# Performance work log

Measured on AMD Instinct MI355X. Metric: run time of the kernel, lower is better.

Reference implementation:

```python
import jax, jax.numpy as jnp
import numpy as np

N = 50000      # total nodes across batch of graphs
E = 800000     # total directed edges (avg degree 16)
B = 64         # number of graphs
D = 128        # input_dim == hidden_dim
L = 4          # num_layers - 1 GIN layers
OUT = 10
BN_EPS = 1e-5


def setup_inputs() -> dict:
    key = jax.random.key(0)
    ks = jax.random.split(key, 12)
    s = 0.05
    return {
        "x": jax.random.normal(ks[0], (N, D), jnp.float32),
        "pi": jax.random.uniform(ks[1], (B, 25), jnp.float32),
        "eps": jnp.zeros((L,), jnp.float32),
        "mlp_w1": jax.random.normal(ks[2], (L, D, D), jnp.float32) * s,
        "mlp_b1": jnp.zeros((L, D), jnp.float32),
        "mlp_bn_g": jnp.ones((L, D), jnp.float32),
        "mlp_bn_b": jnp.zeros((L, D), jnp.float32),
        "mlp_w2": jax.random.normal(ks[3], (L, D, D), jnp.float32) * s,
        "mlp_b2": jnp.zeros((L, D), jnp.float32),
        "bn_g": jnp.ones((L, D), jnp.float32),
        "bn_b": jnp.zeros((L, D), jnp.float32),
        "attend_w": jax.random.normal(ks[4], (D * (L + 1), 1), jnp.float32) * s,
        "attend_b": jnp.zeros((1,), jnp.float32),
        "pi_w": jax.random.normal(ks[5], (25, 16), jnp.float32) * s,
        "pi_b": jnp.zeros((16,), jnp.float32),
        "out_w": jax.random.normal(ks[6], (D * (L + 1) + 16, OUT), jnp.float32) * s,
        "out_b": jnp.zeros((OUT,), jnp.float32),
        "edge_index": jax.random.randint(ks[7], (2, E), 0, N, dtype=jnp.int32),
        "graph_id": jnp.sort(jax.random.randint(ks[8], (N,), 0, B, dtype=jnp.int32)),
    }


def _bn(z, g, b):
    # BatchNorm1d in training mode over all nodes (axis 0)
    m = z.mean(axis=0)
    v = z.var(axis=0)
    return (z - m) * jax.lax.rsqrt(v + BN_EPS) * g + b


def reference(x, pi, eps, mlp_w1, mlp_b1, mlp_bn_g, mlp_bn_b, mlp_w2, mlp_b2,
              bn_g, bn_b, attend_w, attend_b, pi_w, pi_b, out_w, out_b,
              edge_index, graph_id):
    src, dst = edge_index[0], edge_index[1]
    h = x
    reps = [x]
    for l in range(L):
        # GIN sum aggregation (learn_eps=True: no self-loops in Adj)
        pooled = jax.ops.segment_sum(h[src], dst, num_segments=N)
        pooled = pooled + (1.0 + eps[l]) * h
        # 2-layer MLP: Linear -> BN -> ReLU -> Linear
        z = jax.nn.relu(_bn(pooled @ mlp_w1[l] + mlp_b1[l], mlp_bn_g[l], mlp_bn_b[l]))
        z = z @ mlp_w2[l] + mlp_b2[l]
        # outer BN + ReLU
        h = jax.nn.relu(_bn(z, bn_g[l], bn_b[l]))
        reps.append(h)
    hr = jnp.concatenate(reps, axis=1)               # [N, D*(L+1)]
    # per-graph attention softmax over nodes
    scores = (hr @ attend_w + attend_b)[:, 0]        # [N]
    smax = jax.ops.segment_max(scores, graph_id, num_segments=B)
    e = jnp.exp(scores - smax[graph_id])
    denom = jax.ops.segment_sum(e, graph_id, num_segments=B)
    coef = e / denom[graph_id]
    gemb = jax.ops.segment_sum(hr * coef[:, None], graph_id, num_segments=B)  # [B, D*(L+1)]
    # persistence-image branch (PI computed host-side; treated as input)
    pie = jax.nn.relu(pi @ pi_w + pi_b)              # [B, 16]
    feat = jnp.concatenate([gemb, pie], axis=1)      # [B, D*(L+1)+16]
    return feat @ out_w + out_b                      # [B, OUT]
```

## Files before the change

### kernel.cpp

```cpp
#include <hip/hip_runtime.h>
#include <hip/hip_bf16.h>

#define NN 50000
#define EE 800000
#define BBG 64
#define DD 128
#define LLAY 4
#define HRW 640
#define NOUT 10
#define SCANB 196

typedef __hip_bfloat16 bf16;
typedef __attribute__((ext_vector_type(8))) short short8;
typedef __attribute__((ext_vector_type(4))) float f32x4;

__device__ __forceinline__ float b2f(bf16 v) { return __bfloat162float(v); }
__device__ __forceinline__ float bflo(unsigned u) { return __uint_as_float(u << 16); }
__device__ __forceinline__ float bfhi(unsigned u) { return __uint_as_float(u & 0xffff0000u); }
__device__ __forceinline__ unsigned short f2bs(float v) {
  bf16 h = __float2bfloat16(v);
  unsigned short r; __builtin_memcpy(&r, &h, 2); return r;
}
__device__ __forceinline__ int dtype_of(const void* __restrict__ bng) {
  return (*(const unsigned*)bng == 0x3F800000u) ? 1 : 0;
}
__device__ __forceinline__ float ldf(const void* __restrict__ p, long i, int dt) {
  return dt ? ((const float*)p)[i] : b2f(((const bf16*)p)[i]);
}

__device__ __forceinline__ int lower_bound_i(const int* __restrict__ a, int n, int key) {
  int lo = 0, hi = n;
  while (lo < hi) { int mid = (lo + hi) >> 1; if (a[mid] < key) lo = mid + 1; else hi = mid; }
  return lo;
}

__global__ __launch_bounds__(256) void gnn_prep_w(const void* __restrict__ w1,
                                                  const void* __restrict__ w2,
                                                  bf16* __restrict__ w1t,
                                                  bf16* __restrict__ w2t,
                                                  const void* __restrict__ bng) {
  int dt = dtype_of(bng);
  int i = blockIdx.x * 256 + threadIdx.x;
  int l = i >> 14, rem = i & 16383, n = rem >> 7, k = rem & 127;
  long src = (long)l * 16384 + k * 128 + n;
  w1t[i] = __float2bfloat16(ldf(w1, src, dt));
  w2t[i] = __float2bfloat16(ldf(w2, src, dt));
}

__global__ __launch_bounds__(256) void gnn_copy_x(const void* __restrict__ x,
                                                  bf16* __restrict__ hrb,
                                                  const void* __restrict__ bng) {
  int dt = dtype_of(bng);
  int idx = blockIdx.x * 256 + threadIdx.x;
  int n = idx >> 6, cu = idx & 63;
  unsigned o;
  if (dt) {
    const float2 v = ((const float2*)x)[idx];
    o = (unsigned)f2bs(v.x) | ((unsigned)f2bs(v.y) << 16);
  } else {
    o = ((const unsigned*)x)[idx];
  }
  *(unsigned*)(hrb + (size_t)n * HRW + 2 * cu) = o;
}

__global__ __launch_bounds__(256) void gnn_hist(const int* __restrict__ ei,
                                                int* __restrict__ counts,
                                                int* __restrict__ rel) {
  int e = blockIdx.x * 256 + threadIdx.x;
  rel[e] = atomicAdd(&counts[ei[EE + e]], 1);
}

__global__ __launch_bounds__(256) void gnn_scan1(const int* __restrict__ counts,
                                                 int* __restrict__ blocksum) {
  __shared__ int buf[256];
  int tid = threadIdx.x;
  int i = blockIdx.x * 256 + tid;
  buf[tid] = (i < NN) ? counts[i] : 0;
  __syncthreads();
  for (int s = 128; s > 0; s >>= 1) {
    if (tid < s) buf[tid] += buf[tid + s];
    __syncthreads();
  }
  if (tid == 0) blocksum[blockIdx.x] = buf[0];
}

__global__ __launch_bounds__(256) void gnn_scan2(const int* __restrict__ blocksum,
                                                 int* __restrict__ blockofs,
                                                 int* __restrict__ rowstart) {
  __shared__ int buf[256];
  int tid = threadIdx.x;
  int v = (tid < SCANB) ? blocksum[tid] : 0;
  buf[tid] = v;
  __syncthreads();
  for (int ofs = 1; ofs < 256; ofs <<= 1) {
    int t = (tid >= ofs) ? buf[tid - ofs] : 0;
    __syncthreads();
    buf[tid] += t;
    __syncthreads();
  }
  blockofs[tid] = buf[tid] - v;
  if (tid == 255) rowstart[NN] = buf[255];
}

__global__ __launch_bounds__(256) void gnn_scan3(const int* __restrict__ counts,
                                                 const int* __restrict__ blockofs,
                                                 int* __restrict__ rowstart) {
  __shared__ int buf[256];
  int tid = threadIdx.x;
  int i = blockIdx.x * 256 + tid;
  int v = (i < NN) ? counts[i] : 0;
  buf[tid] = v;
  __syncthreads();
  for (int ofs = 1; ofs < 256; ofs <<= 1) {
    int t = (tid >= ofs) ? buf[tid - ofs] : 0;
    __syncthreads();
    buf[tid] += t;
    __syncthreads();
  }
  int val = blockofs[blockIdx.x] + buf[tid] - v;
  if (i < NN) rowstart[i] = val;
}

__global__ __launch_bounds__(256) void gnn_fill(const int* __restrict__ ei,
                                                const int* __restrict__ rowstart,
                                                const int* __restrict__ rel,
                                                int* __restrict__ csr_src) {
  int e = blockIdx.x * 256 + threadIdx.x;
  int src = ei[e];
  int dst = ei[EE + e];
  csr_src[rowstart[dst] + rel[e]] = src;
}

__device__ __forceinline__ void acc8(float* a, uint4 u) {
  a[0] += bflo(u.x); a[1] += bfhi(u.x);
  a[2] += bflo(u.y); a[3] += bfhi(u.y);
  a[4] += bflo(u.z); a[5] += bfhi(u.z);
  a[6] += bflo(u.w); a[7] += bfhi(u.w);
}

__device__ __forceinline__ float2 statsum(const float* __restrict__ stat, int c) {
  float s = 0.f, q = 0.f;
  #pragma unroll
  for (int k = 0; k < 8; k++) { s += stat[k * 256 + c]; q += stat[k * 256 + 128 + c]; }
  return make_float2(s, q);
}

__global__ __launch_bounds__(512) void gnn_gmg1(const bf16* __restrict__ hrb, int l,
                                                const int* __restrict__ rowstart,
                                                const int* __restrict__ csr_src,
                                                const void* __restrict__ eps,
                                                const bf16* __restrict__ Wt,
                                                const void* __restrict__ bias, int biasOfs,
                                                bf16* __restrict__ out,
                                                float* __restrict__ statOut,
                                                const void* __restrict__ bng) {
  int dt = dtype_of(bng);
  __shared__ __align__(16) unsigned ar[16][68];
  int tid = threadIdx.x, w = tid >> 6, lane = tid & 63;
  int q = lane >> 4, il = lane & 15;
  int r0 = blockIdx.x * 16;
  const bf16* stripe = hrb + l * DD;
  float s = 1.0f + ldf(eps, l, dt);

  #pragma unroll
  for (int i = 2 * w; i < 2 * w + 2; i++) {
    int n = r0 + i;
    float a[8] = {0.f, 0.f, 0.f, 0.f, 0.f, 0.f, 0.f, 0.f};
    if (q == 0) {
      uint4 u = *(const uint4*)(stripe + (size_t)n * HRW + il * 8);
      a[0] = s * bflo(u.x); a[1] = s * bfhi(u.x);
      a[2] = s * bflo(u.y); a[3] = s * bfhi(u.y);
      a[4] = s * bflo(u.z); a[5] = s * bfhi(u.z);
      a[6] = s * bflo(u.w); a[7] = s * bfhi(u.w);
    }
    int start = rowstart[n], end = rowstart[n + 1];
    for (int base = start; base < end; base += 64) {
      int m = end - base; if (m > 64) m = 64;
      int idx = (base + lane < end) ? csr_src[base + lane] : 0;
      int j = 0;
      for (; j + 16 <= m; j += 16) {
        int s0 = __shfl(idx, j + q, 64);
        int s1 = __shfl(idx, j + 4 + q, 64);
        int s2 = __shfl(idx, j + 8 + q, 64);
        int s3 = __shfl(idx, j + 12 + q, 64);
        uint4 u0 = *(const uint4*)(stripe + (size_t)s0 * HRW + il * 8);
        uint4 u1 = *(const uint4*)(stripe + (size_t)s1 * HRW + il * 8);
        uint4 u2 = *(const uint4*)(stripe + (size_t)s2 * HRW + il * 8);
        uint4 u3 = *(const uint4*)(stripe + (size_t)s3 * HRW + il * 8);
        acc8(a, u0); acc8(a, u1); acc8(a, u2); acc8(a, u3);
      }
      for (; j + 4 <= m; j += 4) {
        int src = __shfl(idx, j + q, 64);
        uint4 u = *(const uint4*)(stripe + (size_t)src * HRW + il * 8);
        acc8(a, u);
      }
      for (; j < m; j++) {
        int src = __shfl(idx, j, 64);
        if (q == 0) {
          uint4 u = *(const uint4*)(stripe + (size_t)src * HRW + il * 8);
          acc8(a, u);
        }
      }
    }
    #pragma unroll
    for (int k = 0; k < 8; k++) {
      a[k] += __shfl_xor(a[k], 16, 64);
      a[k] += __shfl_xor(a[k], 32, 64);
    }
    if (q == 0) {
      uint4 o;
      o.x = (unsigned)f2bs(a[0]) | ((unsigned)f2bs(a[1]) << 16);
      o.y = (unsigned)f2bs(a[2]) | ((unsigned)f2bs(a[3]) << 16);
      o.z = (unsigned)f2bs(a[4]) | ((unsigned)f2bs(a[5]) << 16);
      o.w = (unsigned)f2bs(a[6]) | ((unsigned)f2bs(a[7]) << 16);
      *(uint4*)&ar[i][il * 4] = o;
    }
  }
  __syncthreads();

  f32x4 acc = (f32x4){0.f, 0.f, 0.f, 0.f};
  #pragma unroll
  for (int ch = 0; ch < 4; ch++) {
    int k0 = ch * 32 + q * 8;
    uint4 raw = *(const uint4*)&ar[il][ch * 16 + q * 4];
    short8 af;
    __builtin_memcpy(&af, &raw, 16);
    short8 bfv = *(const short8*)(Wt + (w * 16 + il) * DD + k0);
    acc = __builtin_amdgcn_mfma_f32_16x16x32_bf16(af, bfv, acc, 0, 0, 0);
  }
  int col = w * 16 + il;
  float bv = ldf(bias, biasOfs + col, dt);
  float ss = 0.f, qq = 0.f;
  #pragma unroll
  for (int r = 0; r < 4; r++) {
    int row = r0 + q * 4 + r;
    float v = acc[r] + bv;
    out[(size_t)row * DD + col] = __float2bfloat16(v);
    ss += v; qq += v * v;
  }
  ss += __shfl_xor(ss, 16, 64);  ss += __shfl_xor(ss, 32, 64);
  qq += __shfl_xor(qq, 16, 64);  qq += __shfl_xor(qq, 32, 64);
  if (q == 0) {
    unsafeAtomicAdd(&statOut[(blockIdx.x & 7) * 256 + col], ss);
    unsafeAtomicAdd(&statOut[(blockIdx.x & 7) * 256 + 128 + col], qq);
  }
}

__global__ __launch_bounds__(256) void gnn_mgemm(const bf16* __restrict__ Abf,
                                                 const bf16* __restrict__ Wt,
                                                 const void* __restrict__ bias, int biasOfs,
                                                 bf16* __restrict__ out,
                                                 const float* __restrict__ statIn,
                                                 const void* __restrict__ g,
                                                 const void* __restrict__ bb, int parOfs,
                                                 float* __restrict__ statOut,
                                                 const void* __restrict__ bng) {
  int dt = dtype_of(bng);
  __shared__ float scf[128], shf[128];
  __shared__ float redS[4][128], redQ[4][128];
  int tid = threadIdx.x, w = tid >> 6, lane = tid & 63;
  int q = lane >> 4, il = lane & 15;
  if (tid < 128) {
    const float invN = 1.0f / NN;
    float2 sq = statsum(statIn, tid);
    float m = sq.x * invN;
    float rs = rsqrtf(sq.y * invN - m * m + 1e-5f);
    float gg = ldf(g, parOfs + tid, dt), bv = ldf(bb, parOfs + tid, dt);
    scf[tid] = rs * gg;
    shf[tid] = bv - m * rs * gg;
  }
  __syncthreads();
  int r0 = (blockIdx.x * 4 + w) * 16;
  int arow = r0 + il;
  int arowc = (arow < NN) ? arow : (NN - 1);
  f32x4 acc[8];
  #pragma unroll
  for (int i = 0; i < 8; i++) acc[i] = (f32x4){0.f, 0.f, 0.f, 0.f};
  #pragma unroll
  for (int ch = 0; ch < 4; ch++) {
    int k0 = ch * 32 + q * 8;
    uint4 raw = *(const uint4*)(Abf + (size_t)arowc * DD + k0);
    float4 c0 = *(const float4*)(scf + k0);
    float4 c1 = *(const float4*)(scf + k0 + 4);
    float4 d0 = *(const float4*)(shf + k0);
    float4 d1 = *(const float4*)(shf + k0 + 4);
    short8 af;
    af[0] = (short)f2bs(fmaxf(bflo(raw.x) * c0.x + d0.x, 0.f));
    af[1] = (short)f2bs(fmaxf(bfhi(raw.x) * c0.y + d0.y, 0.f));
    af[2] = (short)f2bs(fmaxf(bflo(raw.y) * c0.z + d0.z, 0.f));
    af[3] = (short)f2bs(fmaxf(bfhi(raw.y) * c0.w + d0.w, 0.f));
    af[4] = (short)f2bs(fmaxf(bflo(raw.z) * c1.x + d1.x, 0.f));
    af[5] = (short)f2bs(fmaxf(bfhi(raw.z) * c1.y + d1.y, 0.f));
    af[6] = (short)f2bs(fmaxf(bflo(raw.w) * c1.z + d1.z, 0.f));
    af[7] = (short)f2bs(fmaxf(bfhi(raw.w) * c1.w + d1.w, 0.f));
    #pragma unroll
    for (int ct = 0; ct < 8; ct++) {
      short8 bfv = *(const short8*)(Wt + (ct * 16 + il) * DD + k0);
      acc[ct] = __builtin_amdgcn_mfma_f32_16x16x32_bf16(af, bfv, acc[ct], 0, 0, 0);
    }
  }
  #pragma unroll
  for (int ct = 0; ct < 8; ct++) {
    int col = ct * 16 + il;
    float bv = ldf(bias, biasOfs + col, dt);
    float s = 0.f, qq = 0.f;
    #pragma unroll
    for (int r = 0; r < 4; r++) {
      int row = r0 + q * 4 + r;
      float v = acc[ct][r] + bv;
      if (row < NN) {
        out[(size_t)row * DD + col] = __float2bfloat16(v);
        s += v; qq += v * v;
      }
    }
    s += __shfl_xor(s, 16, 64);  s += __shfl_xor(s, 32, 64);
    qq += __shfl_xor(qq, 16, 64); qq += __shfl_xor(qq, 32, 64);
    if (q == 0) { redS[w][col] = s; redQ[w][col] = qq; }
  }
  __syncthreads();
  if (tid < 128) {
    float v = redS[0][tid] + redS[1][tid] + redS[2][tid] + redS[3][tid];
    unsafeAtomicAdd(&statOut[(blockIdx.x & 7) * 256 + tid], v);
  } else {
    int c = tid - 128;
    float v = redQ[0][c] + redQ[1][c] + redQ[2][c] + redQ[3][c];
    unsafeAtomicAdd(&statOut[(blockIdx.x & 7) * 256 + 128 + c], v);
  }
}

__global__ __launch_bounds__(256) void gnn_bn_relu(const bf16* __restrict__ z2,
                                                   const float* __restrict__ stat,
                                                   const void* __restrict__ g,
                                                   const void* __restrict__ bb, int parOfs,
                                                   bf16* __restrict__ hrb, int stripe,
                                                   const void* __restrict__ bng) {
  int dt = dtype_of(bng);
  int cu = threadIdx.x & 63;
  int sub = threadIdx.x >> 6;
  int c0 = 2 * cu, c1 = 2 * cu + 1;
  const float invN = 1.0f / NN;
  float2 sqa = statsum(stat, c0);
  float2 sqb = statsum(stat, c1);
  float m0 = sqa.x * invN, m1 = sqb.x * invN;
  float sc0 = rsqrtf(sqa.y * invN - m0 * m0 + 1e-5f) * ldf(g, parOfs + c0, dt);
  float sc1 = rsqrtf(sqb.y * invN - m1 * m1 + 1e-5f) * ldf(g, parOfs + c1, dt);
  float sh0 = ldf(bb, parOfs + c0, dt) - m0 * sc0;
  float sh1 = ldf(bb, parOfs + c1, dt) - m1 * sc1;
  for (int r = blockIdx.x * 4 + sub; r < NN; r += 2048) {
    unsigned u = *(const unsigned*)(z2 + (size_t)r * DD + c0);
    float v0 = fmaxf(bflo(u) * sc0 + sh0, 0.f);
    float v1 = fmaxf(bfhi(u) * sc1 + sh1, 0.f);
    *(unsigned*)(hrb + (size_t)r * HRW + stripe * DD + c0) =
        (unsigned)f2bs(v0) | ((unsigned)f2bs(v1) << 16);
  }
}

__global__ __launch_bounds__(256) void gnn_scores(const bf16* __restrict__ hrb,
                                                  const void* __restrict__ aw,
                                                  const void* __restrict__ ab,
                                                  float* __restrict__ scores,
                                                  const void* __restrict__ bng) {
  int dt = dtype_of(bng);
  int w = threadIdx.x >> 6;
  int lane = threadIdx.x & 63;
  int n = blockIdx.x * 4 + w;
  const unsigned* rowp = (const unsigned*)(hrb + (size_t)n * HRW);
  float s = 0.f;
  #pragma unroll
  for (int i = 0; i < 5; i++) {
    int c2 = lane + i * 64;
    unsigned u = rowp[c2];
    s += bflo(u) * ldf(aw, 2 * c2, dt) + bfhi(u) * ldf(aw, 2 * c2 + 1, dt);
  }
  #pragma unroll
  for (int m = 32; m > 0; m >>= 1) s += __shfl_xor(s, m, 64);
  if (lane == 0) scores[n] = s + ldf(ab, 0, dt);
}

__global__ __launch_bounds__(256) void gnn_softmax(float* __restrict__ scores,
                                                   const int* __restrict__ gid) {
  int b = blockIdx.x;
  int tid = threadIdx.x;
  int start = lower_bound_i(gid, NN, b);
  int end = lower_bound_i(gid, NN, b + 1);
  __shared__ float red[256];
  float mx = -3.4e38f;
  for (int n = start + tid; n < end; n += 256) mx = fmaxf(mx, scores[n]);
  red[tid] = mx;
  __syncthreads();
  for (int s = 128; s > 0; s >>= 1) {
    if (tid < s) red[tid] = fmaxf(red[tid], red[tid + s]);
    __syncthreads();
  }
  float smax = red[0];
  __syncthreads();
  float sum = 0.f;
  for (int n = start + tid; n < end; n += 256) sum += expf(scores[n] - smax);
  red[tid] = sum;
  __syncthreads();
  for (int s = 128; s > 0; s >>= 1) {
    if (tid < s) red[tid] += red[tid + s];
    __syncthreads();
  }
  float denom = red[0];
  float inv = (denom > 0.f) ? 1.0f / denom : 0.f;
  for (int n = start + tid; n < end; n += 256) scores[n] = expf(scores[n] - smax) * inv;
}

__global__ __launch_bounds__(128) void gnn_gemb(const bf16* __restrict__ hrb,
                                                const float* __restrict__ coef,
                                                const int* __restrict__ gid,
                                                float* __restrict__ gemb) {
  int b = blockIdx.x / 40;
  int part = blockIdx.x % 40;
  int chunk = part % 5;
  int slice = part / 5;
  int c = chunk * 128 + threadIdx.x;
  int start = lower_bound_i(gid, NN, b);
  int end = lower_bound_i(gid, NN, b + 1);
  float acc = 0.f;
  for (int n = start + slice; n < end; n += 8)
    acc += b2f(hrb[(size_t)n * HRW + c]) * coef[n];
  unsafeAtomicAdd(&gemb[b * HRW + c], acc);
}

__global__ __launch_bounds__(64) void gnn_final(const float* __restrict__ gemb,
                                                const void* __restrict__ pi,
                                                const void* __restrict__ piw,
                                                const void* __restrict__ pib,
                                                const void* __restrict__ ow,
                                                const void* __restrict__ ob,
                                                void* __restrict__ out,
                                                const void* __restrict__ bng) {
  int dt = dtype_of(bng);
  int b = blockIdx.x;
  int t = threadIdx.x;
  __shared__ float pie[16];
  if (t < 16) {
    float s = ldf(pib, t, dt);
    for (int i = 0; i < 25; i++) s += ldf(pi, b * 25 + i, dt) * ldf(piw, i * 16 + t, dt);
    pie[t] = fmaxf(s, 0.f);
  }
  __syncthreads();
  for (int o = 0; o < NOUT; o++) {
    float s = 0.f;
    for (int c = t; c < HRW + 16; c += 64) {
      float f = (c < HRW) ? gemb[b * HRW + c] : pie[c - HRW];
      s += f * ldf(ow, c * NOUT + o, dt);
    }
    #pragma unroll
    for (int m = 32; m > 0; m >>= 1) s += __shfl_xor(s, m, 64);
    if (t == 0) {
      float r = s + ldf(ob, o, dt);
      if (dt) ((float*)out)[b * NOUT + o] = r;
      else ((bf16*)out)[b * NOUT + o] = __float2bfloat16(r);
    }
  }
}

extern "C" void kernel_launch(void* const* d_in, const int* in_sizes, int n_in,
                              void* d_out, int out_size, void* d_ws, size_t ws_size,
                              hipStream_t stream) {
  const void* x    = d_in[0];
  const void* pi   = d_in[1];
  const void* eps  = d_in[2];
  const void* w1   = d_in[3];
  const void* b1   = d_in[4];
  const void* bng  = d_in[5];
  const void* bnb  = d_in[6];
  const void* w2   = d_in[7];
  const void* b2   = d_in[8];
  const void* obng = d_in[9];
  const void* obnb = d_in[10];
  const void* aw   = d_in[11];
  const void* ab   = d_in[12];
  const void* piw  = d_in[13];
  const void* pib  = d_in[14];
  const void* ow   = d_in[15];
  const void* ob   = d_in[16];
  const int*  ei   = (const int*)d_in[17];
  const int*  gid  = (const int*)d_in[18];

  bf16*  hrb      = (bf16*)d_ws;
  bf16*  z1       = hrb + (size_t)NN * HRW;
  bf16*  z2       = z1 + (size_t)NN * DD;
  bf16*  w1t      = z2 + (size_t)NN * DD;
  bf16*  w2t      = w1t + LLAY * DD * DD;
  float* statbufs = (float*)(w2t + LLAY * DD * DD);
  float* gemb     = statbufs + 8 * 2048;
  int*   counts   = (int*)(gemb + BBG * HRW);
  size_t zeroBytes = (size_t)(8 * 2048 + BBG * HRW) * 4 + (size_t)NN * 4;
  int*   rowstart = counts + NN;
  int*   rel      = rowstart + NN + 1;
  int*   csr_src  = rel + EE;
  int*   blocksum = csr_src + EE;
  int*   blockofs = blocksum + 256;
  float* scores   = (float*)(blockofs + 256);

  hipMemsetAsync(statbufs, 0, zeroBytes, stream);
  gnn_prep_w<<<256, 256, 0, stream>>>(w1, w2, w1t, w2t, bng);
  gnn_copy_x<<<12500, 256, 0, stream>>>(x, hrb, bng);

  gnn_hist<<<EE / 256, 256, 0, stream>>>(ei, counts, rel);
  gnn_scan1<<<SCANB, 256, 0, stream>>>(counts, blocksum);
  gnn_scan2<<<1, 256, 0, stream>>>(blocksum, blockofs, rowstart);
  gnn_scan3<<<SCANB, 256, 0, stream>>>(counts, blockofs, rowstart);
  gnn_fill<<<EE / 256, 256, 0, stream>>>(ei, rowstart, rel, csr_src);

  for (int l = 0; l < LLAY; l++) {
    float* statA = statbufs + (l * 2 + 0) * 2048;
    float* statB = statbufs + (l * 2 + 1) * 2048;
    gnn_gmg1<<<NN / 16, 512, 0, stream>>>(hrb, l, rowstart, csr_src, eps,
                                          w1t + l * DD * DD, b1, l * DD,
                                          z1, statA, bng);
    gnn_mgemm<<<782, 256, 0, stream>>>(z1, w2t + l * DD * DD, b2, l * DD,
                                       z2, statA, bng, bnb, l * DD,
                                       statB, bng);
    gnn_bn_relu<<<512, 256, 0, stream>>>(z2, statB, obng, obnb, l * DD,
                                         hrb, l + 1, bng);
  }

  gnn_scores<<<12500, 256, 0, stream>>>(hrb, aw, ab, scores, bng);
  gnn_softmax<<<BBG, 256, 0, stream>>>(scores, gid);
  gnn_gemb<<<BBG * 40, 128, 0, stream>>>(hrb, scores, gid, gemb);
  gnn_final<<<BBG, 64, 0, stream>>>(gemb, pi, piw, pib, ow, ob, d_out, bng);
}
```

Measured before the change: 585.5 us.

## Fuse attention scoring into init/BN kernels and softmax into gemb; merge scans

Computes the attention score contributions incrementally, accumulating atomically per node in the x-copy kernel and in each layer's BN+ReLU kernel, which removes the separate full re-read of the 640-wide hr matrix. The softmax is folded into the gemb kernel: each block recomputes its graph's max and sum, so the standalone softmax kernel goes away. The weight prep and x copy are merged into one launch, and the two-pass scan offset kernel is removed by having each block sum the preceding block totals itself. An 8-wide gather tail is added. The trade-offs are redundant softmax reductions across 40 blocks per graph, extra atomics on scores, and the attention bias being dropped, which cancels in the softmax.

```diff
diff --git a/kernel.cpp b/kernel.cpp
--- a/kernel.cpp
+++ b/kernel.cpp
@@ -34,33 +34,51 @@
   return lo;
 }
 
-__global__ __launch_bounds__(256) void gnn_prep_w(const void* __restrict__ w1,
-                                                  const void* __restrict__ w2,
-                                                  bf16* __restrict__ w1t,
-                                                  bf16* __restrict__ w2t,
-                                                  const void* __restrict__ bng) {
+__global__ __launch_bounds__(256) void gnn_init(const void* __restrict__ x,
+                                                bf16* __restrict__ hrb,
+                                                const void* __restrict__ w1,
+                                                const void* __restrict__ w2,
+                                                bf16* __restrict__ w1t,
+                                                bf16* __restrict__ w2t,
+                                                const void* __restrict__ aw,
+                                                float* __restrict__ scores,
+                                                const void* __restrict__ bng) {
   int dt = dtype_of(bng);
-  int i = blockIdx.x * 256 + threadIdx.x;
-  int l = i >> 14, rem = i & 16383, n = rem >> 7, k = rem & 127;
-  long src = (long)l * 16384 + k * 128 + n;
-  w1t[i] = __float2bfloat16(ldf(w1, src, dt));
-  w2t[i] = __float2bfloat16(ldf(w2, src, dt));
-}
-
-__global__ __launch_bounds__(256) void gnn_copy_x(const void* __restrict__ x,
-                                                  bf16* __restrict__ hrb,
-                                                  const void* __restrict__ bng) {
-  int dt = dtype_of(bng);
-  int idx = blockIdx.x * 256 + threadIdx.x;
-  int n = idx >> 6, cu = idx & 63;
-  unsigned o;
+  int tid = threadIdx.x;
+  if (blockIdx.x >= 3125) {
+    int i = (blockIdx.x - 3125) * 256 + tid;
+    int l = i >> 14, rem = i & 16383, n = rem >> 7, k = rem & 127;
+    long src = (long)l * 16384 + k * 128 + n;
+    w1t[i] = __float2bfloat16(ldf(w1, src, dt));
+    w2t[i] = __float2bfloat16(ldf(w2, src, dt));
+    return;
+  }
+  int n = blockIdx.x * 16 + (tid >> 4);
+  int il = tid & 15;
+  long base = (long)n * DD + il * 8;
+  float v[8];
   if (dt) {
-    const float2 v = ((const float2*)x)[idx];
-    o = (unsigned)f2bs(v.x) | ((unsigned)f2bs(v.y) << 16);
+    float4 a0 = *(const float4*)((const float*)x + base);
+    float4 a1 = *(const float4*)((const float*)x + base + 4);
+    v[0] = a0.x; v[1] = a0.y; v[2] = a0.z; v[3] = a0.w;
+    v[4] = a1.x; v[5] = a1.y; v[6] = a1.z; v[7] = a1.w;
   } else {
-    o = ((const unsigned*)x)[idx];
-  }
-  *(unsigned*)(hrb + (size_t)n * HRW + 2 * cu) = o;
+    uint4 u = *(const uint4*)((const bf16*)x + base);
+    v[0] = bflo(u.x); v[1] = bfhi(u.x); v[2] = bflo(u.y); v[3] = bfhi(u.y);
+    v[4] = bflo(u.z); v[5] = bfhi(u.z); v[6] = bflo(u.w); v[7] = bfhi(u.w);
+  }
+  uint4 o;
+  o.x = (unsigned)f2bs(v[0]) | ((unsigned)f2bs(v[1]) << 16);
+  o.y = (unsigned)f2bs(v[2]) | ((unsigned)f2bs(v[3]) << 16);
+  o.z = (unsigned)f2bs(v[4]) | ((unsigned)f2bs(v[5]) << 16);
+  o.w = (unsigned)f2bs(v[6]) | ((unsigned)f2bs(v[7]) << 16);
+  *(uint4*)(hrb + (size_t)n * HRW + il * 8) = o;
+  float ss = 0.f;
+  #pragma unroll
+  for (int k = 0; k < 8; k++) ss += v[k] * ldf(aw, il * 8 + k, dt);
+  ss += __shfl_xor(ss, 1, 64); ss += __shfl_xor(ss, 2, 64);
+  ss += __shfl_xor(ss, 4, 64); ss += __shfl_xor(ss, 8, 64);
+  if (il == 0) unsafeAtomicAdd(&scores[n], ss);
 }
 
 __global__ __launch_bounds__(256) void gnn_hist(const int* __restrict__ ei,
@@ -84,12 +102,23 @@
   if (tid == 0) blocksum[blockIdx.x] = buf[0];
 }
 
-__global__ __launch_bounds__(256) void gnn_scan2(const int* __restrict__ blocksum,
-                                                 int* __restrict__ blockofs,
+__global__ __launch_bounds__(256) void gnn_scan3(const int* __restrict__ counts,
+                                                 const int* __restrict__ blocksum,
                                                  int* __restrict__ rowstart) {
   __shared__ int buf[256];
   int tid = threadIdx.x;
-  int v = (tid < SCANB) ? blocksum[tid] : 0;
+  int partial = 0;
+  for (int i = tid; i < blockIdx.x; i += 256) partial += blocksum[i];
+  buf[tid] = partial;
+  __syncthreads();
+  for (int s = 128; s > 0; s >>= 1) {
+    if (tid < s) buf[tid] += buf[tid + s];
+    __syncthreads();
+  }
+  int offset = buf[0];
+  __syncthreads();
+  int i = blockIdx.x * 256 + tid;
+  int v = (i < NN) ? counts[i] : 0;
   buf[tid] = v;
   __syncthreads();
   for (int ofs = 1; ofs < 256; ofs <<= 1) {
@@ -98,27 +127,9 @@
     buf[tid] += t;
     __syncthreads();
   }
-  blockofs[tid] = buf[tid] - v;
-  if (tid == 255) rowstart[NN] = buf[255];
-}
-
-__global__ __launch_bounds__(256) void gnn_scan3(const int* __restrict__ counts,
-                                                 const int* __restrict__ blockofs,
-                                                 int* __restrict__ rowstart) {
-  __shared__ int buf[256];
-  int tid = threadIdx.x;
-  int i = blockIdx.x * 256 + tid;
-  int v = (i < NN) ? counts[i] : 0;
-  buf[tid] = v;
-  __syncthreads();
-  for (int ofs = 1; ofs < 256; ofs <<= 1) {
-    int t = (tid >= ofs) ? buf[tid - ofs] : 0;
-    __syncthreads();
-    buf[tid] += t;
-    __syncthreads();
-  }
-  int val = blockofs[blockIdx.x] + buf[tid] - v;
+  int val = offset + buf[tid] - v;
   if (i < NN) rowstart[i] = val;
+  if (blockIdx.x == SCANB - 1 && tid == 255) rowstart[NN] = offset + buf[255];
 }
 
 __global__ __launch_bounds__(256) void gnn_fill(const int* __restrict__ ei,
@@ -188,6 +199,13 @@
         uint4 u2 = *(const uint4*)(stripe + (size_t)s2 * HRW + il * 8);
         uint4 u3 = *(const uint4*)(stripe + (size_t)s3 * HRW + il * 8);
         acc8(a, u0); acc8(a, u1); acc8(a, u2); acc8(a, u3);
+      }
+      for (; j + 8 <= m; j += 8) {
+        int s0 = __shfl(idx, j + q, 64);
+        int s1 = __shfl(idx, j + 4 + q, 64);
+        uint4 u0 = *(const uint4*)(stripe + (size_t)s0 * HRW + il * 8);
+        uint4 u1 = *(const uint4*)(stripe + (size_t)s1 * HRW + il * 8);
+        acc8(a, u0); acc8(a, u1);
       }
       for (; j + 4 <= m; j += 4) {
         int src = __shfl(idx, j + q, 64);
@@ -333,94 +351,83 @@
                                                    const void* __restrict__ g,
                                                    const void* __restrict__ bb, int parOfs,
                                                    bf16* __restrict__ hrb, int stripe,
+                                                   const void* __restrict__ aw,
+                                                   float* __restrict__ scores,
                                                    const void* __restrict__ bng) {
   int dt = dtype_of(bng);
-  int cu = threadIdx.x & 63;
-  int sub = threadIdx.x >> 6;
-  int c0 = 2 * cu, c1 = 2 * cu + 1;
-  const float invN = 1.0f / NN;
-  float2 sqa = statsum(stat, c0);
-  float2 sqb = statsum(stat, c1);
-  float m0 = sqa.x * invN, m1 = sqb.x * invN;
-  float sc0 = rsqrtf(sqa.y * invN - m0 * m0 + 1e-5f) * ldf(g, parOfs + c0, dt);
-  float sc1 = rsqrtf(sqb.y * invN - m1 * m1 + 1e-5f) * ldf(g, parOfs + c1, dt);
-  float sh0 = ldf(bb, parOfs + c0, dt) - m0 * sc0;
-  float sh1 = ldf(bb, parOfs + c1, dt) - m1 * sc1;
-  for (int r = blockIdx.x * 4 + sub; r < NN; r += 2048) {
-    unsigned u = *(const unsigned*)(z2 + (size_t)r * DD + c0);
-    float v0 = fmaxf(bflo(u) * sc0 + sh0, 0.f);
-    float v1 = fmaxf(bfhi(u) * sc1 + sh1, 0.f);
-    *(unsigned*)(hrb + (size_t)r * HRW + stripe * DD + c0) =
-        (unsigned)f2bs(v0) | ((unsigned)f2bs(v1) << 16);
-  }
-}
-
-__global__ __launch_bounds__(256) void gnn_scores(const bf16* __restrict__ hrb,
-                                                  const void* __restrict__ aw,
-                                                  const void* __restrict__ ab,
-                                                  float* __restrict__ scores,
-                                                  const void* __restrict__ bng) {
-  int dt = dtype_of(bng);
-  int w = threadIdx.x >> 6;
-  int lane = threadIdx.x & 63;
-  int n = blockIdx.x * 4 + w;
-  const unsigned* rowp = (const unsigned*)(hrb + (size_t)n * HRW);
-  float s = 0.f;
-  #pragma unroll
-  for (int i = 0; i < 5; i++) {
-    int c2 = lane + i * 64;
-    unsigned u = rowp[c2];
-    s += bflo(u) * ldf(aw, 2 * c2, dt) + bfhi(u) * ldf(aw, 2 * c2 + 1, dt);
-  }
-  #pragma unroll
-  for (int m = 32; m > 0; m >>= 1) s += __shfl_xor(s, m, 64);
-  if (lane == 0) scores[n] = s + ldf(ab, 0, dt);
-}
-
-__global__ __launch_bounds__(256) void gnn_softmax(float* __restrict__ scores,
-                                                   const int* __restrict__ gid) {
-  int b = blockIdx.x;
+  __shared__ float scf[128], shf[128], awf[128];
   int tid = threadIdx.x;
-  int start = lower_bound_i(gid, NN, b);
-  int end = lower_bound_i(gid, NN, b + 1);
-  __shared__ float red[256];
-  float mx = -3.4e38f;
-  for (int n = start + tid; n < end; n += 256) mx = fmaxf(mx, scores[n]);
-  red[tid] = mx;
-  __syncthreads();
-  for (int s = 128; s > 0; s >>= 1) {
-    if (tid < s) red[tid] = fmaxf(red[tid], red[tid + s]);
-    __syncthreads();
-  }
-  float smax = red[0];
-  __syncthreads();
-  float sum = 0.f;
-  for (int n = start + tid; n < end; n += 256) sum += expf(scores[n] - smax);
-  red[tid] = sum;
-  __syncthreads();
-  for (int s = 128; s > 0; s >>= 1) {
-    if (tid < s) red[tid] += red[tid + s];
-    __syncthreads();
-  }
-  float denom = red[0];
-  float inv = (denom > 0.f) ? 1.0f / denom : 0.f;
-  for (int n = start + tid; n < end; n += 256) scores[n] = expf(scores[n] - smax) * inv;
+  if (tid < 128) {
+    const float invN = 1.0f / NN;
+    float2 sq = statsum(stat, tid);
+    float m = sq.x * invN;
+    float rs = rsqrtf(sq.y * invN - m * m + 1e-5f);
+    float gg = ldf(g, parOfs + tid, dt), bv = ldf(bb, parOfs + tid, dt);
+    scf[tid] = rs * gg;
+    shf[tid] = bv - m * rs * gg;
+    awf[tid] = ldf(aw, stripe * DD + tid, dt);
+  }
+  __syncthreads();
+  int n = blockIdx.x * 16 + (tid >> 4);
+  int il = tid & 15;
+  int c0 = il * 8;
+  uint4 u = *(const uint4*)(z2 + (size_t)n * DD + c0);
+  float v[8];
+  v[0] = bflo(u.x); v[1] = bfhi(u.x); v[2] = bflo(u.y); v[3] = bfhi(u.y);
+  v[4] = bflo(u.z); v[5] = bfhi(u.z); v[6] = bflo(u.w); v[7] = bfhi(u.w);
+  float ss = 0.f;
+  #pragma unroll
+  for (int k = 0; k < 8; k++) {
+    v[k] = fmaxf(v[k] * scf[c0 + k] + shf[c0 + k], 0.f);
+    ss += v[k] * awf[c0 + k];
+  }
+  uint4 o;
+  o.x = (unsigned)f2bs(v[0]) | ((unsigned)f2bs(v[1]) << 16);
+  o.y = (unsigned)f2bs(v[2]) | ((unsigned)f2bs(v[3]) << 16);
+  o.z = (unsigned)f2bs(v[4]) | ((unsigned)f2bs(v[5]) << 16);
+  o.w = (unsigned)f2bs(v[6]) | ((unsigned)f2bs(v[7]) << 16);
+  *(uint4*)(hrb + (size_t)n * HRW + stripe * DD + c0) = o;
+  ss += __shfl_xor(ss, 1, 64); ss += __shfl_xor(ss, 2, 64);
+  ss += __shfl_xor(ss, 4, 64); ss += __shfl_xor(ss, 8, 64);
+  if (il == 0) unsafeAtomicAdd(&scores[n], ss);
 }
 
 __global__ __launch_bounds__(128) void gnn_gemb(const bf16* __restrict__ hrb,
-                                                const float* __restrict__ coef,
+                                                const float* __restrict__ scores,
                                                 const int* __restrict__ gid,
                                                 float* __restrict__ gemb) {
   int b = blockIdx.x / 40;
   int part = blockIdx.x % 40;
   int chunk = part % 5;
   int slice = part / 5;
-  int c = chunk * 128 + threadIdx.x;
+  int tid = threadIdx.x;
   int start = lower_bound_i(gid, NN, b);
   int end = lower_bound_i(gid, NN, b + 1);
+  __shared__ float red[128];
+  float mx = -3.4e38f;
+  for (int n = start + tid; n < end; n += 128) mx = fmaxf(mx, scores[n]);
+  red[tid] = mx;
+  __syncthreads();
+  for (int s = 64; s > 0; s >>= 1) {
+    if (tid < s) red[tid] = fmaxf(red[tid], red[tid + s]);
+    __syncthreads();
+  }
+  float smax = red[0];
+  __syncthreads();
+  float sum = 0.f;
+  for (int n = start + tid; n < end; n += 128) sum += __expf(scores[n] - smax);
+  red[tid] = sum;
+  __syncthreads();
+  for (int s = 64; s > 0; s >>= 1) {
+    if (tid < s) red[tid] += red[tid + s];
+    __syncthreads();
+  }
+  float denom = red[0];
+  float inv = (denom > 0.f) ? 1.0f / denom : 0.f;
+  int c = chunk * 128 + tid;
   float acc = 0.f;
   for (int n = start + slice; n < end; n += 8)
-    acc += b2f(hrb[(size_t)n * HRW + c]) * coef[n];
+    acc += b2f(hrb[(size_t)n * HRW + c]) * __expf(scores[n] - smax) * inv;
   unsafeAtomicAdd(&gemb[b * HRW + c], acc);
 }
 
@@ -473,7 +480,6 @@
   const void* obng = d_in[9];
   const void* obnb = d_in[10];
   const void* aw   = d_in[11];
-  const void* ab   = d_in[12];
   const void* piw  = d_in[13];
   const void* pib  = d_in[14];
   const void* ow   = d_in[15];
@@ -489,22 +495,19 @@
   float* statbufs = (float*)(w2t + LLAY * DD * DD);
   float* gemb     = statbufs + 8 * 2048;
   int*   counts   = (int*)(gemb + BBG * HRW);
-  size_t zeroBytes = (size_t)(8 * 2048 + BBG * HRW) * 4 + (size_t)NN * 4;
-  int*   rowstart = counts + NN;
+  float* scores   = (float*)(counts + NN);
+  size_t zeroBytes = (size_t)(8 * 2048 + BBG * HRW + NN + NN) * 4;
+  int*   rowstart = (int*)(scores + NN);
   int*   rel      = rowstart + NN + 1;
   int*   csr_src  = rel + EE;
   int*   blocksum = csr_src + EE;
-  int*   blockofs = blocksum + 256;
-  float* scores   = (float*)(blockofs + 256);
 
   hipMemsetAsync(statbufs, 0, zeroBytes, stream);
-  gnn_prep_w<<<256, 256, 0, stream>>>(w1, w2, w1t, w2t, bng);
-  gnn_copy_x<<<12500, 256, 0, stream>>>(x, hrb, bng);
+  gnn_init<<<3381, 256, 0, stream>>>(x, hrb, w1, w2, w1t, w2t, aw, scores, bng);
 
   gnn_hist<<<EE / 256, 256, 0, stream>>>(ei, counts, rel);
   gnn_scan1<<<SCANB, 256, 0, stream>>>(counts, blocksum);
-  gnn_scan2<<<1, 256, 0, stream>>>(blocksum, blockofs, rowstart);
-  gnn_scan3<<<SCANB, 256, 0, stream>>>(counts, blockofs, rowstart);
+  gnn_scan3<<<SCANB, 256, 0, stream>>>(counts, blocksum, rowstart);
   gnn_fill<<<EE / 256, 256, 0, stream>>>(ei, rowstart, rel, csr_src);
 
   for (int l = 0; l < LLAY; l++) {
@@ -516,12 +519,10 @@
     gnn_mgemm<<<782, 256, 0, stream>>>(z1, w2t + l * DD * DD, b2, l * DD,
                                        z2, statA, bng, bnb, l * DD,
                                        statB, bng);
-    gnn_bn_relu<<<512, 256, 0, stream>>>(z2, statB, obng, obnb, l * DD,
-                                         hrb, l + 1, bng);
-  }
-
-  gnn_scores<<<12500, 256, 0, stream>>>(hrb, aw, ab, scores, bng);
-  gnn_softmax<<<BBG, 256, 0, stream>>>(scores, gid);
+    gnn_bn_relu<<<NN / 16, 256, 0, stream>>>(z2, statB, obng, obnb, l * DD,
+                                             hrb, l + 1, aw, scores, bng);
+  }
+
   gnn_gemb<<<BBG * 40, 128, 0, stream>>>(hrb, scores, gid, gemb);
   gnn_final<<<BBG, 64, 0, stream>>>(gemb, pi, piw, pib, ow, ob, d_out, bng);
 }
```

Result: faster. 554.5 us (-5.3%).
